# Kernel optimization log

Measured on AMD Instinct MI355X. Metric: run time of the kernel, lower is better.

The kernel has to match this reference:

```python
import jax, jax.numpy as jnp
import numpy as np

D_MODEL = 256
NUM_UNIVERSES = 8
D_UNIVERSE = D_MODEL // NUM_UNIVERSES
B, S = 1, 1024
TEMP = 5.0
NEG = -1e9


def setup_inputs() -> dict:
    key = jax.random.key(0)
    ks = jax.random.split(key, 5)
    scale = 1.0 / np.sqrt(D_MODEL)
    return {
        "x": jax.random.normal(ks[0], (B, S, D_MODEL), dtype=jnp.float32),
        "Wq": jax.random.normal(ks[1], (D_MODEL, D_MODEL), dtype=jnp.float32) * scale,
        "bq": jnp.zeros((D_MODEL,), dtype=jnp.float32),
        "Wk": jax.random.normal(ks[2], (D_MODEL, D_MODEL), dtype=jnp.float32) * scale,
        "bk": jnp.zeros((D_MODEL,), dtype=jnp.float32),
        "Wv": jax.random.normal(ks[3], (D_MODEL, D_MODEL), dtype=jnp.float32) * scale,
        "bv": jnp.zeros((D_MODEL,), dtype=jnp.float32),
        "Wo": jax.random.normal(ks[4], (D_MODEL, D_MODEL), dtype=jnp.float32) * scale,
        "bo": jnp.zeros((D_MODEL,), dtype=jnp.float32),
    }


def reference(x, Wq, bq, Wk, bk, Wv, bv, Wo, bo):
    b, s, d = x.shape
    h, du = NUM_UNIVERSES, D_UNIVERSE
    # Projections; Q,K squashed to [0,1] fuzzy truth values
    Q = jax.nn.sigmoid(x @ Wq + bq)
    K = jax.nn.sigmoid(x @ Wk + bk)
    V = x @ Wv + bv
    # [B,S,D] -> [B,H,S,du]
    Q = Q.reshape(b, s, h, du).transpose(0, 2, 1, 3)
    K = K.reshape(b, s, h, du).transpose(0, 2, 1, 3)
    V = V.reshape(b, s, h, du).transpose(0, 2, 1, 3)
    # Fuzzy implication: clamp(1 - Q_i + K_j, max=1), mean over d_universe
    # Broadcast to [B,H,S,S,du] (the memory-heavy intermediate)
    implication = jnp.minimum(1.0 - Q[:, :, :, None, :] + K[:, :, None, :, :], 1.0)
    truth = implication.mean(axis=-1)  # [B,H,S,S]
    # Causal mask
    causal = jnp.tril(jnp.ones((s, s), dtype=bool))
    truth = jnp.where(causal[None, None], truth, NEG)
    attn = jax.nn.softmax(truth * TEMP, axis=-1)
    out = jnp.einsum("bhij,bhjd->bhid", attn, V)
    out = out.transpose(0, 2, 1, 3).reshape(b, s, d)
    return out @ Wo + bo
```

## Files before the change

kernel.cpp:

```cpp
#include <hip/hip_runtime.h>
#include <hip/hip_bf16.h>
#include <math.h>

#define S_LEN 1024
#define DM    256
#define DU    32
#define TEMPF 5.0f
#define NS    4

typedef float f32x4  __attribute__((ext_vector_type(4)));
typedef short bf16x8 __attribute__((ext_vector_type(8)));

__device__ __forceinline__ unsigned short f32_to_bf16_rne(float x) {
    unsigned int b = __float_as_uint(x);
    b += 0x7FFFu + ((b >> 16) & 1u);
    return (unsigned short)(b >> 16);
}

__device__ __forceinline__ void split_bf16(float f, unsigned short& h, unsigned short& l) {
    h = f32_to_bf16_rne(f);
    float hf = __uint_as_float((unsigned int)h << 16);
    l = f32_to_bf16_rne(f - hf);
}

__global__ __launch_bounds__(256) void qkv_proj_kernel(
    const float* __restrict__ x,
    const float* __restrict__ Wq, const float* __restrict__ bq,
    const float* __restrict__ Wk, const float* __restrict__ bk,
    const float* __restrict__ Wv, const float* __restrict__ bv,
    float* __restrict__ qo, float* __restrict__ ko, float* __restrict__ vo)
{
    const int n0g = blockIdx.x * 64;
    const int mat = n0g >> 8;
    const int n0  = n0g & 255;
    const float* __restrict__ W    = (mat == 0) ? Wq : ((mat == 1) ? Wk : Wv);
    const float* __restrict__ bias = (mat == 0) ? bq : ((mat == 1) ? bk : bv);
    float* __restrict__ dst        = (mat == 0) ? qo : ((mat == 1) ? ko : vo);

    const int m0   = blockIdx.y * 64;
    const int t    = threadIdx.x;
    const int w    = t >> 6;
    const int lane = t & 63;
    const int fm   = lane & 15;
    const int quad = lane >> 4;
    const int q8   = quad * 8;

    __shared__ __align__(16) unsigned short Ah[2][64][40], Al[2][64][40];
    __shared__ __align__(16) unsigned short Bh[2][64][40], Bl[2][64][40];

    const int xr  = t >> 2;
    const int xf  = (t & 3) * 8;
    const int wn  = t & 63;
    const int wkc = (t >> 6) * 8;

    f32x4 acc[4];
    #pragma unroll
    for (int nt = 0; nt < 4; nt++)
        #pragma unroll
        for (int i = 0; i < 4; i++) acc[nt][i] = 0.0f;

    const float* xbase = x + (m0 + xr) * DM + xf;
    float xa[8], wv[8];

    {
        float4 a0 = *(const float4*)xbase;
        float4 a1 = *(const float4*)(xbase + 4);
        xa[0]=a0.x; xa[1]=a0.y; xa[2]=a0.z; xa[3]=a0.w;
        xa[4]=a1.x; xa[5]=a1.y; xa[6]=a1.z; xa[7]=a1.w;
        #pragma unroll
        for (int i = 0; i < 8; i++) wv[i] = W[(wkc + i) * DM + n0 + wn];
    }
    {
        bf16x8 vh, vl;
        #pragma unroll
        for (int i = 0; i < 8; i++) { unsigned short h,l; split_bf16(xa[i],h,l); vh[i]=(short)h; vl[i]=(short)l; }
        *(bf16x8*)&Ah[0][xr][xf] = vh; *(bf16x8*)&Al[0][xr][xf] = vl;
        #pragma unroll
        for (int i = 0; i < 8; i++) { unsigned short h,l; split_bf16(wv[i],h,l); vh[i]=(short)h; vl[i]=(short)l; }
        *(bf16x8*)&Bh[0][wn][wkc] = vh; *(bf16x8*)&Bl[0][wn][wkc] = vl;
    }
    __syncthreads();

    int buf = 0;
    for (int step = 0; step < 8; step++) {
        if (step < 7) {
            const float* xp = xbase + (step + 1) * 32;
            float4 a0 = *(const float4*)xp;
            float4 a1 = *(const float4*)(xp + 4);
            xa[0]=a0.x; xa[1]=a0.y; xa[2]=a0.z; xa[3]=a0.w;
            xa[4]=a1.x; xa[5]=a1.y; xa[6]=a1.z; xa[7]=a1.w;
            #pragma unroll
            for (int i = 0; i < 8; i++)
                wv[i] = W[((step + 1) * 32 + wkc + i) * DM + n0 + wn];
        }
        {
            bf16x8 ah = *(const bf16x8*)&Ah[buf][16 * w + fm][q8];
            bf16x8 al = *(const bf16x8*)&Al[buf][16 * w + fm][q8];
            #pragma unroll
            for (int nt = 0; nt < 4; nt++) {
                bf16x8 bh = *(const bf16x8*)&Bh[buf][nt * 16 + fm][q8];
                bf16x8 bl = *(const bf16x8*)&Bl[buf][nt * 16 + fm][q8];
                acc[nt] = __builtin_amdgcn_mfma_f32_16x16x32_bf16(ah, bh, acc[nt], 0, 0, 0);
                acc[nt] = __builtin_amdgcn_mfma_f32_16x16x32_bf16(al, bh, acc[nt], 0, 0, 0);
                acc[nt] = __builtin_amdgcn_mfma_f32_16x16x32_bf16(ah, bl, acc[nt], 0, 0, 0);
            }
        }
        if (step < 7) {
            const int nb = buf ^ 1;
            bf16x8 vh, vl;
            #pragma unroll
            for (int i = 0; i < 8; i++) { unsigned short h,l; split_bf16(xa[i],h,l); vh[i]=(short)h; vl[i]=(short)l; }
            *(bf16x8*)&Ah[nb][xr][xf] = vh; *(bf16x8*)&Al[nb][xr][xf] = vl;
            #pragma unroll
            for (int i = 0; i < 8; i++) { unsigned short h,l; split_bf16(wv[i],h,l); vh[i]=(short)h; vl[i]=(short)l; }
            *(bf16x8*)&Bh[nb][wn][wkc] = vh; *(bf16x8*)&Bl[nb][wn][wkc] = vl;
            __syncthreads();
            buf = nb;
        }
    }

    #pragma unroll
    for (int nt = 0; nt < 4; nt++) {
        const int col = n0 + nt * 16 + fm;
        const float bb = bias[col];
        const int hh = col >> 5;
        const int dd = col & 31;
        float* dp = dst + hh * (S_LEN * DU) + dd;
        #pragma unroll
        for (int reg = 0; reg < 4; reg++) {
            const int row = m0 + 16 * w + quad * 4 + reg;
            float val = acc[nt][reg] + bb;
            if (mat < 2) val = 1.0f / (1.0f + __expf(-val));
            dp[row * DU] = val;
        }
    }
}

__global__ __launch_bounds__(256, 2) void attn_kernel(
    const float* __restrict__ q, const float* __restrict__ k,
    const float* __restrict__ v,
    float* __restrict__ part_o, float* __restrict__ part_l)
{
    const int bid = blockIdx.x;
    const int it4 = 15 - (bid >> 5);
    const int sub = bid & 31;
    const int h   = sub & 7;
    const int s   = sub >> 3;
    const int t   = threadIdx.x;
    const int r   = t >> 4;
    const int c   = t & 15;
    const int w   = t >> 6;
    const int i0  = it4 * 64;

    __shared__ __align__(16) float          Ks[64][36];
    __shared__ __align__(16) unsigned short Vt[32][88];
    __shared__ __align__(16) unsigned short Ps[64][88];

    float qreg[4][32];
    #pragma unroll
    for (int kq = 0; kq < 4; kq++) {
        const float* qrow = q + h * (S_LEN * DU) + (i0 + r + 16 * kq) * DU;
        #pragma unroll
        for (int d4 = 0; d4 < 8; d4++) {
            float4 qv = *(const float4*)&qrow[d4 * 4];
            qreg[kq][d4*4+0] = qv.x; qreg[kq][d4*4+1] = qv.y;
            qreg[kq][d4*4+2] = qv.z; qreg[kq][d4*4+3] = qv.w;
        }
    }

    float lpart[4] = {0.0f, 0.0f, 0.0f, 0.0f};
    f32x4 acc0 = {0.0f, 0.0f, 0.0f, 0.0f};
    f32x4 acc1 = {0.0f, 0.0f, 0.0f, 0.0f};

    const int jr = t >> 2;
    const int d0 = (t & 3) * 8;
    const float* kbase = k + h * (S_LEN * DU);
    const float* vbase = v + h * (S_LEN * DU);

    const int lane = t & 63;
    const int m    = lane & 15;
    const int quad = lane >> 4;

    const int njt = it4 + 1;
    float4 ka, kb, va, vb;
    if (s < njt) {
        const float* kp = kbase + (s * 64 + jr) * DU + d0;
        const float* vp = vbase + (s * 64 + jr) * DU + d0;
        ka = *(const float4*)kp; kb = *(const float4*)(kp + 4);
        va = *(const float4*)vp; vb = *(const float4*)(vp + 4);
    }

    for (int jt = s; jt < njt; jt += NS) {
        __syncthreads();
        *(float4*)&Ks[jr][d0]     = ka;
        *(float4*)&Ks[jr][d0 + 4] = kb;
        {
            float vv[8] = {va.x, va.y, va.z, va.w, vb.x, vb.y, vb.z, vb.w};
            #pragma unroll
            for (int i = 0; i < 8; i++)
                Vt[d0 + i][jr] = f32_to_bf16_rne(vv[i]);
        }
        __syncthreads();
        if (jt + NS < njt) {
            const float* kp = kbase + ((jt + NS) * 64 + jr) * DU + d0;
            const float* vp = vbase + ((jt + NS) * 64 + jr) * DU + d0;
            ka = *(const float4*)kp; kb = *(const float4*)(kp + 4);
            va = *(const float4*)vp; vb = *(const float4*)(vp + 4);
        }

        #pragma unroll
        for (int q4 = 0; q4 < 4; q4++) {
            const int jj  = c + q4 * 16;
            const int jgl = jt * 64 + jj;
            float sacc[4] = {0.0f, 0.0f, 0.0f, 0.0f};
            #pragma unroll
            for (int d = 0; d < 32; d += 4) {
                float4 k4 = *(const float4*)&Ks[jj][d];
                #pragma unroll
                for (int kq = 0; kq < 4; kq++) {
                    sacc[kq] += fmaxf(qreg[kq][d+0] - k4.x, 0.0f)
                              + fmaxf(qreg[kq][d+1] - k4.y, 0.0f)
                              + fmaxf(qreg[kq][d+2] - k4.z, 0.0f)
                              + fmaxf(qreg[kq][d+3] - k4.w, 0.0f);
                }
            }
            #pragma unroll
            for (int kq = 0; kq < 4; kq++) {
                const int ig = i0 + r + 16 * kq;
                const float p = (jgl <= ig)
                    ? __expf(TEMPF - (TEMPF / 32.0f) * sacc[kq]) : 0.0f;
                lpart[kq] += p;
                Ps[r + 16 * kq][jj] = f32_to_bf16_rne(p);
            }
        }
        __syncthreads();

        #pragma unroll
        for (int kc = 0; kc < 2; kc++) {
            bf16x8 a  = *(const bf16x8*)&Ps[16 * w + m][kc * 32 + quad * 8];
            bf16x8 b0 = *(const bf16x8*)&Vt[m]     [kc * 32 + quad * 8];
            bf16x8 b1 = *(const bf16x8*)&Vt[m + 16][kc * 32 + quad * 8];
            acc0 = __builtin_amdgcn_mfma_f32_16x16x32_bf16(a, b0, acc0, 0, 0, 0);
            acc1 = __builtin_amdgcn_mfma_f32_16x16x32_bf16(a, b1, acc1, 0, 0, 0);
        }
    }

    #pragma unroll
    for (int off = 8; off; off >>= 1)
        #pragma unroll
        for (int kq = 0; kq < 4; kq++)
            lpart[kq] += __shfl_xor(lpart[kq], off, 16);

    const int pbase = (h * 16 + it4) * NS + s;
    float* po = part_o + (size_t)pbase * 2048;
    #pragma unroll
    for (int reg = 0; reg < 4; reg++) {
        const int row = 16 * w + quad * 4 + reg;
        po[row * 32 + m]      = acc0[reg];
        po[row * 32 + m + 16] = acc1[reg];
    }
    if (c == 0) {
        #pragma unroll
        for (int kq = 0; kq < 4; kq++)
            part_l[pbase * 64 + r + 16 * kq] = lpart[kq];
    }
}

__global__ __launch_bounds__(256) void out_proj_kernel(
    const float* __restrict__ part_o, const float* __restrict__ part_l,
    const float* __restrict__ W, const float* __restrict__ bias,
    float* __restrict__ dst)
{
    const int n0  = blockIdx.x * 64;
    const int it4 = blockIdx.y;
    const int m0  = it4 * 64;
    const int t    = threadIdx.x;
    const int w    = t >> 6;
    const int lane = t & 63;
    const int fm   = lane & 15;
    const int quad = lane >> 4;
    const int q8   = quad * 8;

    __shared__ __align__(16) unsigned short Ah[2][64][40], Al[2][64][40];
    __shared__ __align__(16) unsigned short Bh[2][64][40], Bl[2][64][40];

    const int xr  = t >> 2;
    const int xf  = (t & 3) * 8;
    const int wn  = t & 63;
    const int wkc = (t >> 6) * 8;

    f32x4 acc[4];
    #pragma unroll
    for (int nt = 0; nt < 4; nt++)
        #pragma unroll
        for (int i = 0; i < 4; i++) acc[nt][i] = 0.0f;

    float xa[8], wv[8];

    auto loadA = [&](int h) {
        const int base = (h * 16 + it4) * NS;
        float o[8] = {0,0,0,0,0,0,0,0};
        float l = 0.0f;
        #pragma unroll
        for (int s2 = 0; s2 < NS; s2++) {
            const float* po = part_o + (size_t)(base + s2) * 2048 + xr * 32 + xf;
            float4 p0 = *(const float4*)po;
            float4 p1 = *(const float4*)(po + 4);
            o[0]+=p0.x; o[1]+=p0.y; o[2]+=p0.z; o[3]+=p0.w;
            o[4]+=p1.x; o[5]+=p1.y; o[6]+=p1.z; o[7]+=p1.w;
            l += part_l[(base + s2) * 64 + xr];
        }
        const float inv = 1.0f / l;
        #pragma unroll
        for (int i = 0; i < 8; i++) xa[i] = o[i] * inv;
    };
    auto loadW = [&](int k0) {
        #pragma unroll
        for (int i = 0; i < 8; i++) wv[i] = W[(k0 + wkc + i) * DM + n0 + wn];
    };
    auto storeT = [&](int b) {
        bf16x8 vh, vl;
        #pragma unroll
        for (int i = 0; i < 8; i++) { unsigned short h,l; split_bf16(xa[i],h,l); vh[i]=(short)h; vl[i]=(short)l; }
        *(bf16x8*)&Ah[b][xr][xf] = vh; *(bf16x8*)&Al[b][xr][xf] = vl;
        #pragma unroll
        for (int i = 0; i < 8; i++) { unsigned short h,l; split_bf16(wv[i],h,l); vh[i]=(short)h; vl[i]=(short)l; }
        *(bf16x8*)&Bh[b][wn][wkc] = vh; *(bf16x8*)&Bl[b][wn][wkc] = vl;
    };

    loadA(0); loadW(0);
    storeT(0);
    __syncthreads();

    int buf = 0;
    for (int step = 0; step < 8; step++) {
        if (step < 7) { loadA(step + 1); loadW((step + 1) * 32); }
        {
            bf16x8 ah = *(const bf16x8*)&Ah[buf][16 * w + fm][q8];
            bf16x8 al = *(const bf16x8*)&Al[buf][16 * w + fm][q8];
            #pragma unroll
            for (int nt = 0; nt < 4; nt++) {
                bf16x8 bh = *(const bf16x8*)&Bh[buf][nt * 16 + fm][q8];
                bf16x8 bl = *(const bf16x8*)&Bl[buf][nt * 16 + fm][q8];
                acc[nt] = __builtin_amdgcn_mfma_f32_16x16x32_bf16(ah, bh, acc[nt], 0, 0, 0);
                acc[nt] = __builtin_amdgcn_mfma_f32_16x16x32_bf16(al, bh, acc[nt], 0, 0, 0);
                acc[nt] = __builtin_amdgcn_mfma_f32_16x16x32_bf16(ah, bl, acc[nt], 0, 0, 0);
            }
        }
        if (step < 7) {
            const int nb = buf ^ 1;
            storeT(nb);
            __syncthreads();
            buf = nb;
        }
    }

    #pragma unroll
    for (int nt = 0; nt < 4; nt++) {
        const int col = n0 + nt * 16 + fm;
        const float bb = bias[col];
        #pragma unroll
        for (int reg = 0; reg < 4; reg++) {
            const int row = m0 + 16 * w + quad * 4 + reg;
            dst[row * DM + col] = acc[nt][reg] + bb;
        }
    }
}

extern "C" void kernel_launch(void* const* d_in, const int* in_sizes, int n_in,
                              void* d_out, int out_size, void* d_ws, size_t ws_size,
                              hipStream_t stream)
{
    const float* x  = (const float*)d_in[0];
    const float* Wq = (const float*)d_in[1];
    const float* bq = (const float*)d_in[2];
    const float* Wk = (const float*)d_in[3];
    const float* bk = (const float*)d_in[4];
    const float* Wv = (const float*)d_in[5];
    const float* bv = (const float*)d_in[6];
    const float* Wo = (const float*)d_in[7];
    const float* bo = (const float*)d_in[8];
    float* out = (float*)d_out;

    float* ws      = (float*)d_ws;
    float* q       = ws;
    float* k       = q + 262144;
    float* v       = k + 262144;
    float* part_o  = v + 262144;
    float* part_l  = part_o + 1048576;

    qkv_proj_kernel<<<dim3(12, 16), 256, 0, stream>>>(x, Wq, bq, Wk, bk, Wv, bv, q, k, v);
    attn_kernel<<<dim3(512), 256, 0, stream>>>(q, k, v, part_o, part_l);
    out_proj_kernel<<<dim3(4, 16), 256, 0, stream>>>(part_o, part_l, Wo, bo, out);
}
```

Before: 109.2 us.

## Compute fuzzy implication scores in packed fp16 and narrow out-proj tiles

The attention score loop now holds Q and K in fp16 and uses packed half subtract and max, then fdot2 with ones to accumulate each pair into an fp32 sum. This roughly halves the VALU instruction count and register and LDS footprint of the inner product-like loop, at the cost of fp16 rounding of sigmoid outputs in [0,1]. Separately, the output projection tile width drops from 64 to 32 columns, doubling the grid to 128 blocks for better CU coverage while repeating the partial-sum combine per block.

New measurement: 107.1 us (median of 2 runs). About the same (-1.9%).

```diff
diff --git a/kernel.cpp b/kernel.cpp
--- a/kernel.cpp
+++ b/kernel.cpp
@@ -8,8 +8,10 @@
 #define TEMPF 5.0f
 #define NS    4
 
-typedef float f32x4  __attribute__((ext_vector_type(4)));
-typedef short bf16x8 __attribute__((ext_vector_type(8)));
+typedef float    f32x4  __attribute__((ext_vector_type(4)));
+typedef short    bf16x8 __attribute__((ext_vector_type(8)));
+typedef _Float16 f16x2  __attribute__((ext_vector_type(2)));
+typedef _Float16 f16x8  __attribute__((ext_vector_type(8)));
 
 __device__ __forceinline__ unsigned short f32_to_bf16_rne(float x) {
     unsigned int b = __float_as_uint(x);
@@ -152,21 +154,23 @@
     const int w   = t >> 6;
     const int i0  = it4 * 64;
 
-    __shared__ __align__(16) float          Ks[64][36];
+    __shared__ __align__(16) _Float16       Kh[64][40];
     __shared__ __align__(16) unsigned short Vt[32][88];
     __shared__ __align__(16) unsigned short Ps[64][88];
 
-    float qreg[4][32];
+    f16x2 qh[4][16];
     #pragma unroll
     for (int kq = 0; kq < 4; kq++) {
         const float* qrow = q + h * (S_LEN * DU) + (i0 + r + 16 * kq) * DU;
         #pragma unroll
         for (int d4 = 0; d4 < 8; d4++) {
             float4 qv = *(const float4*)&qrow[d4 * 4];
-            qreg[kq][d4*4+0] = qv.x; qreg[kq][d4*4+1] = qv.y;
-            qreg[kq][d4*4+2] = qv.z; qreg[kq][d4*4+3] = qv.w;
-        }
-    }
+            qh[kq][d4*2+0] = (f16x2){(_Float16)qv.x, (_Float16)qv.y};
+            qh[kq][d4*2+1] = (f16x2){(_Float16)qv.z, (_Float16)qv.w};
+        }
+    }
+    const f16x2 one2  = {(_Float16)1.0f, (_Float16)1.0f};
+    const f16x2 zero2 = {(_Float16)0.0f, (_Float16)0.0f};
 
     float lpart[4] = {0.0f, 0.0f, 0.0f, 0.0f};
     f32x4 acc0 = {0.0f, 0.0f, 0.0f, 0.0f};
@@ -192,9 +196,12 @@
 
     for (int jt = s; jt < njt; jt += NS) {
         __syncthreads();
-        *(float4*)&Ks[jr][d0]     = ka;
-        *(float4*)&Ks[jr][d0 + 4] = kb;
         {
+            float kv[8] = {ka.x, ka.y, ka.z, ka.w, kb.x, kb.y, kb.z, kb.w};
+            f16x8 kh8;
+            #pragma unroll
+            for (int i = 0; i < 8; i++) kh8[i] = (_Float16)kv[i];
+            *(f16x8*)&Kh[jr][d0] = kh8;
             float vv[8] = {va.x, va.y, va.z, va.w, vb.x, vb.y, vb.z, vb.w};
             #pragma unroll
             for (int i = 0; i < 8; i++)
@@ -214,14 +221,21 @@
             const int jgl = jt * 64 + jj;
             float sacc[4] = {0.0f, 0.0f, 0.0f, 0.0f};
             #pragma unroll
-            for (int d = 0; d < 32; d += 4) {
-                float4 k4 = *(const float4*)&Ks[jj][d];
+            for (int d8 = 0; d8 < 4; d8++) {
+                f16x8 k8 = *(const f16x8*)&Kh[jj][d8 * 8];
                 #pragma unroll
-                for (int kq = 0; kq < 4; kq++) {
-                    sacc[kq] += fmaxf(qreg[kq][d+0] - k4.x, 0.0f)
-                              + fmaxf(qreg[kq][d+1] - k4.y, 0.0f)
-                              + fmaxf(qreg[kq][d+2] - k4.z, 0.0f)
-                              + fmaxf(qreg[kq][d+3] - k4.w, 0.0f);
+                for (int p2 = 0; p2 < 4; p2++) {
+                    f16x2 kk = {k8[2*p2], k8[2*p2+1]};
+                    #pragma unroll
+                    for (int kq = 0; kq < 4; kq++) {
+                        f16x2 diff = qh[kq][d8*4+p2] - kk;
+                        f16x2 mx = __builtin_elementwise_max(diff, zero2);
+#if defined(__has_builtin) && __has_builtin(__builtin_amdgcn_fdot2)
+                        sacc[kq] = __builtin_amdgcn_fdot2(mx, one2, sacc[kq], false);
+#else
+                        sacc[kq] += (float)mx[0] + (float)mx[1];
+#endif
+                    }
                 }
             }
             #pragma unroll
@@ -271,7 +285,7 @@
     const float* __restrict__ W, const float* __restrict__ bias,
     float* __restrict__ dst)
 {
-    const int n0  = blockIdx.x * 64;
+    const int n0  = blockIdx.x * 32;
     const int it4 = blockIdx.y;
     const int m0  = it4 * 64;
     const int t    = threadIdx.x;
@@ -282,20 +296,20 @@
     const int q8   = quad * 8;
 
     __shared__ __align__(16) unsigned short Ah[2][64][40], Al[2][64][40];
-    __shared__ __align__(16) unsigned short Bh[2][64][40], Bl[2][64][40];
+    __shared__ __align__(16) unsigned short Bh[2][32][40], Bl[2][32][40];
 
     const int xr  = t >> 2;
     const int xf  = (t & 3) * 8;
-    const int wn  = t & 63;
-    const int wkc = (t >> 6) * 8;
-
-    f32x4 acc[4];
-    #pragma unroll
-    for (int nt = 0; nt < 4; nt++)
+    const int wn  = t & 31;
+    const int wkb = (t >> 5) * 4;
+
+    f32x4 acc[2];
+    #pragma unroll
+    for (int nt = 0; nt < 2; nt++)
         #pragma unroll
         for (int i = 0; i < 4; i++) acc[nt][i] = 0.0f;
 
-    float xa[8], wv[8];
+    float xa[8], wv[4];
 
     auto loadA = [&](int h) {
         const int base = (h * 16 + it4) * NS;
@@ -316,16 +330,21 @@
     };
     auto loadW = [&](int k0) {
         #pragma unroll
-        for (int i = 0; i < 8; i++) wv[i] = W[(k0 + wkc + i) * DM + n0 + wn];
+        for (int i = 0; i < 4; i++) wv[i] = W[(k0 + wkb + i) * DM + n0 + wn];
     };
     auto storeT = [&](int b) {
         bf16x8 vh, vl;
         #pragma unroll
         for (int i = 0; i < 8; i++) { unsigned short h,l; split_bf16(xa[i],h,l); vh[i]=(short)h; vl[i]=(short)l; }
         *(bf16x8*)&Ah[b][xr][xf] = vh; *(bf16x8*)&Al[b][xr][xf] = vl;
-        #pragma unroll
-        for (int i = 0; i < 8; i++) { unsigned short h,l; split_bf16(wv[i],h,l); vh[i]=(short)h; vl[i]=(short)l; }
-        *(bf16x8*)&Bh[b][wn][wkc] = vh; *(bf16x8*)&Bl[b][wn][wkc] = vl;
+        ushort4 bh4, bl4;
+        unsigned short hh, ll;
+        split_bf16(wv[0], hh, ll); bh4.x = hh; bl4.x = ll;
+        split_bf16(wv[1], hh, ll); bh4.y = hh; bl4.y = ll;
+        split_bf16(wv[2], hh, ll); bh4.z = hh; bl4.z = ll;
+        split_bf16(wv[3], hh, ll); bh4.w = hh; bl4.w = ll;
+        *(ushort4*)&Bh[b][wn][wkb] = bh4;
+        *(ushort4*)&Bl[b][wn][wkb] = bl4;
     };
 
     loadA(0); loadW(0);
@@ -339,7 +358,7 @@
             bf16x8 ah = *(const bf16x8*)&Ah[buf][16 * w + fm][q8];
             bf16x8 al = *(const bf16x8*)&Al[buf][16 * w + fm][q8];
             #pragma unroll
-            for (int nt = 0; nt < 4; nt++) {
+            for (int nt = 0; nt < 2; nt++) {
                 bf16x8 bh = *(const bf16x8*)&Bh[buf][nt * 16 + fm][q8];
                 bf16x8 bl = *(const bf16x8*)&Bl[buf][nt * 16 + fm][q8];
                 acc[nt] = __builtin_amdgcn_mfma_f32_16x16x32_bf16(ah, bh, acc[nt], 0, 0, 0);
@@ -356,7 +375,7 @@
     }
 
     #pragma unroll
-    for (int nt = 0; nt < 4; nt++) {
+    for (int nt = 0; nt < 2; nt++) {
         const int col = n0 + nt * 16 + fm;
         const float bb = bias[col];
         #pragma unroll
@@ -391,5 +410,5 @@
 
     qkv_proj_kernel<<<dim3(12, 16), 256, 0, stream>>>(x, Wq, bq, Wk, bk, Wv, bv, q, k, v);
     attn_kernel<<<dim3(512), 256, 0, stream>>>(q, k, v, part_o, part_l);
-    out_proj_kernel<<<dim3(4, 16), 256, 0, stream>>>(part_o, part_l, Wo, bo, out);
-}
+    out_proj_kernel<<<dim3(8, 16), 256, 0, stream>>>(part_o, part_l, Wo, bo, out);
+}
```
